# Optimization experiments

Measured on AMD Instinct MI355X. Metric: run time of the kernel, lower is better.

The kernel has to match this reference:

```python
import jax, jax.numpy as jnp
import numpy as np

HEAD_DIM = 128
NUM_QUERY_GROUPS = 4
BLOCK_SIZE = 64
NUM_SELECTED = 16


def setup_inputs() -> dict:
    key = jax.random.key(0)
    k1, k2, k3, k4 = jax.random.split(key, 4)
    query = jax.random.normal(k1, (4, 32, 1, 128), jnp.float32)
    compressed_keys = jax.random.normal(k2, (4, 32, 128, 128), jnp.float32)
    keys = jax.random.normal(k3, (4, 4, 8192, 128), jnp.float32)
    values = jax.random.normal(k4, (4, 4, 8192, 128), jnp.float32)
    return {"query": query, "compressed_keys": compressed_keys, "keys": keys, "values": values}


def reference(query, compressed_keys, keys, values):
    # --- compressed attention importance scores ---
    q = query[:, :, -1, :]                                     # [B, H, D] (last query position)
    scale = 1.0 / (HEAD_DIM ** 0.5)
    scores = jnp.einsum('bhd,bhnd->bhn', q, compressed_keys) * scale  # [B, H, N]
    probs = jax.nn.softmax(scores, axis=-1)
    # --- GQA pooling: mean over heads within each query group ---
    B, H, N = probs.shape
    probs = probs.reshape(B, NUM_QUERY_GROUPS, H // NUM_QUERY_GROUPS, N).mean(axis=2)  # [B, G, N]
    # --- top-k block selection ---
    _, idx = jax.lax.top_k(probs, NUM_SELECTED)                # [B, G, n]
    block_starts = idx * BLOCK_SIZE                            # [B, G, n]
    offsets = jnp.arange(BLOCK_SIZE, dtype=block_starts.dtype)
    gather_idx = (block_starts[..., None] + offsets).reshape(B, NUM_QUERY_GROUPS, NUM_SELECTED * BLOCK_SIZE)  # [B, G, n*bs]
    # --- gather whole K/V blocks ---
    selected_keys = jnp.take_along_axis(keys, gather_idx[..., None], axis=2)    # [B, G, n*bs, D]
    selected_values = jnp.take_along_axis(values, gather_idx[..., None], axis=2)
    return selected_keys, selected_values
```

## Files before the change

kernel.cpp:

```cpp
#include <hip/hip_runtime.h>
#include <math.h>

#define BB   4
#define HH   32
#define GG   4
#define HPG  8
#define DD   128
#define NCK  128
#define SEQ  8192
#define NSEL 16
#define BLK  64

__global__ __launch_bounds__(512, 1) void gemv_exp_kernel(const float* __restrict__ query,
                                                          const float* __restrict__ ck,
                                                          float* __restrict__ e_out,
                                                          float* __restrict__ psum_out) {
    const int blk  = blockIdx.x;
    const int bh   = blk >> 1;
    const int half = blk & 1;
    const int t    = threadIdx.x;
    const int r    = (t >> 3) + half * 64;
    const int sub  = t & 7;
    const int w    = t >> 6;

    __shared__ float q_sh[DD];
    __shared__ float wred[8];

    if (t < DD) q_sh[t] = query[(size_t)bh * DD + t];
    __syncthreads();

    const float4* c4 = (const float4*)(ck + ((size_t)bh * NCK + r) * DD) + sub;
    const float4* q4 = ((const float4*)q_sh) + sub;
    float s = 0.0f;
    #pragma unroll
    for (int i = 0; i < 4; ++i) {
        float4 a = q4[i * 8];
        float4 c = c4[i * 8];
        s += a.x * c.x + a.y * c.y + a.z * c.z + a.w * c.w;
    }
    s += __shfl_xor(s, 1);
    s += __shfl_xor(s, 2);
    s += __shfl_xor(s, 4);

    const float e = expf(s * 0.08838834764831845f);
    if (sub == 0) e_out[(size_t)bh * NCK + r] = e;

    float bsum = e;
    #pragma unroll
    for (int off = 1; off < 64; off <<= 1) bsum += __shfl_xor(bsum, off);
    if ((t & 63) == 0) wred[w] = bsum * 0.125f;
    __syncthreads();

    if (t == 0) {
        float p = 0.0f;
        #pragma unroll
        for (int i = 0; i < 8; ++i) p += wred[i];
        psum_out[bh * 2 + half] = p;
    }
}

__global__ __launch_bounds__(256, 1) void select_gather_kernel(const float* __restrict__ e_in,
                                                               const float* __restrict__ psum,
                                                               const float* __restrict__ keys,
                                                               const float* __restrict__ values,
                                                               float* __restrict__ out) {
    const int bid  = blockIdx.x;
    const int q2   = bid & 3;
    const int isV  = q2 >> 1;
    const int half = q2 & 1;
    const int s    = (bid >> 2) & 15;
    const int bg   = bid >> 6;
    const int b    = bg >> 2;
    const int g    = bg & 3;
    const int t    = threadIdx.x;

    __shared__ float pm[NCK];
    __shared__ int   sel_sh;

    if (t < NCK) {
        const int base = b * HH + g * HPG;
        float p = 0.0f;
        #pragma unroll
        for (int j = 0; j < HPG; ++j) {
            const float ej = e_in[(size_t)(base + j) * NCK + t];
            const float sj = psum[(base + j) * 2] + psum[(base + j) * 2 + 1];
            p += ej / sj;
        }
        pm[t] = p;
    }
    __syncthreads();

    if (t < NCK) {
        const float mv = pm[t];
        int rank = 0;
        for (int i = 0; i < NCK; ++i) {
            const float vi = pm[i];
            if (vi > mv || (vi == mv && i < t)) ++rank;
        }
        if (rank == s) sel_sh = t;
    }
    __syncthreads();
    const int sel = sel_sh;

    const size_t src  = ((size_t)bg * SEQ + (size_t)sel * BLK + half * 32) * DD;
    const size_t dst  = ((size_t)bg * (NSEL * BLK) + (size_t)s * BLK + half * 32) * DD;
    const size_t VOFF = (size_t)BB * GG * NSEL * BLK * DD;

    const float4* sp = (const float4*)((isV ? values : keys) + src);
    float4*       dp = (float4*)(out + (isV ? VOFF : 0) + dst);

    #pragma unroll
    for (int i = 0; i < 4; ++i) dp[i * 256 + t] = sp[i * 256 + t];
}

extern "C" void kernel_launch(void* const* d_in, const int* in_sizes, int n_in,
                              void* d_out, int out_size, void* d_ws, size_t ws_size,
                              hipStream_t stream) {
    const float* query  = (const float*)d_in[0];
    const float* ck     = (const float*)d_in[1];
    const float* keys   = (const float*)d_in[2];
    const float* values = (const float*)d_in[3];
    float* out = (float*)d_out;

    float* e_ws   = (float*)d_ws;
    float* ps_ws  = (float*)((char*)d_ws + (size_t)BB * HH * NCK * sizeof(float));

    gemv_exp_kernel<<<BB * HH * 2, 512, 0, stream>>>(query, ck, e_ws, ps_ws);
    select_gather_kernel<<<BB * GG * NSEL * 4, 256, 0, stream>>>(e_ws, ps_ws, keys, values, out);
}
```

Before: 18.45 us.

## Fuse score and gather kernels with a global atomic grid barrier

```diff
diff --git a/kernel.cpp b/kernel.cpp
--- a/kernel.cpp
+++ b/kernel.cpp
@@ -10,61 +10,72 @@
 #define SEQ  8192
 #define NSEL 16
 #define BLK  64
+#define NPROD 256
 
-__global__ __launch_bounds__(512, 1) void gemv_exp_kernel(const float* __restrict__ query,
-                                                          const float* __restrict__ ck,
-                                                          float* __restrict__ e_out,
-                                                          float* __restrict__ psum_out) {
-    const int blk  = blockIdx.x;
-    const int bh   = blk >> 1;
-    const int half = blk & 1;
-    const int t    = threadIdx.x;
-    const int r    = (t >> 3) + half * 64;
-    const int sub  = t & 7;
-    const int w    = t >> 6;
+__global__ __launch_bounds__(256, 4) void fused_nsa_kernel(
+    const float* __restrict__ query,
+    const float* __restrict__ ck,
+    const float* __restrict__ keys,
+    const float* __restrict__ values,
+    float* __restrict__ e_ws,
+    float* __restrict__ ps_ws,
+    unsigned int* __restrict__ ctr,
+    float* __restrict__ out)
+{
+    const int bid = blockIdx.x;
+    const int t   = threadIdx.x;
 
     __shared__ float q_sh[DD];
-    __shared__ float wred[8];
+    __shared__ float wred[4];
+    __shared__ float pm[NCK];
+    __shared__ int   sel_sh;
 
-    if (t < DD) q_sh[t] = query[(size_t)bh * DD + t];
+    if (bid < NPROD) {
+        const int bh   = bid >> 1;
+        const int half = bid & 1;
+        const int r    = half * 64 + (t >> 2);
+        const int sub  = t & 3;
+        const int w    = t >> 6;
+
+        if (t < DD) q_sh[t] = query[(size_t)bh * DD + t];
+        __syncthreads();
+
+        const float4* c4 = (const float4*)(ck + ((size_t)bh * NCK + r) * DD) + sub;
+        const float4* q4 = ((const float4*)q_sh) + sub;
+        float s = 0.0f;
+        #pragma unroll
+        for (int i = 0; i < 8; ++i) {
+            float4 a = q4[i * 4];
+            float4 c = c4[i * 4];
+            s += a.x * c.x + a.y * c.y + a.z * c.z + a.w * c.w;
+        }
+        s += __shfl_xor(s, 1);
+        s += __shfl_xor(s, 2);
+
+        const float e = expf(s * 0.08838834764831845f);
+        if (sub == 0) e_ws[(size_t)bh * NCK + r] = e;
+
+        float bsum = e;
+        #pragma unroll
+        for (int off = 1; off < 64; off <<= 1) bsum += __shfl_xor(bsum, off);
+        if ((t & 63) == 0) wred[w] = bsum * 0.25f;
+        __syncthreads();
+        if (t == 0)
+            ps_ws[bh * 2 + half] = (wred[0] + wred[1]) + (wred[2] + wred[3]);
+
+        __threadfence();
+        __syncthreads();
+        if (t == 0)
+            __hip_atomic_fetch_add(ctr, 1u, __ATOMIC_RELEASE, __HIP_MEMORY_SCOPE_AGENT);
+    }
+
+    if (t == 0) {
+        while (__hip_atomic_load(ctr, __ATOMIC_RELAXED, __HIP_MEMORY_SCOPE_AGENT) != NPROD)
+            __builtin_amdgcn_s_sleep(2);
+        (void)__hip_atomic_load(ctr, __ATOMIC_ACQUIRE, __HIP_MEMORY_SCOPE_AGENT);
+    }
     __syncthreads();
 
-    const float4* c4 = (const float4*)(ck + ((size_t)bh * NCK + r) * DD) + sub;
-    const float4* q4 = ((const float4*)q_sh) + sub;
-    float s = 0.0f;
-    #pragma unroll
-    for (int i = 0; i < 4; ++i) {
-        float4 a = q4[i * 8];
-        float4 c = c4[i * 8];
-        s += a.x * c.x + a.y * c.y + a.z * c.z + a.w * c.w;
-    }
-    s += __shfl_xor(s, 1);
-    s += __shfl_xor(s, 2);
-    s += __shfl_xor(s, 4);
-
-    const float e = expf(s * 0.08838834764831845f);
-    if (sub == 0) e_out[(size_t)bh * NCK + r] = e;
-
-    float bsum = e;
-    #pragma unroll
-    for (int off = 1; off < 64; off <<= 1) bsum += __shfl_xor(bsum, off);
-    if ((t & 63) == 0) wred[w] = bsum * 0.125f;
-    __syncthreads();
-
-    if (t == 0) {
-        float p = 0.0f;
-        #pragma unroll
-        for (int i = 0; i < 8; ++i) p += wred[i];
-        psum_out[bh * 2 + half] = p;
-    }
-}
-
-__global__ __launch_bounds__(256, 1) void select_gather_kernel(const float* __restrict__ e_in,
-                                                               const float* __restrict__ psum,
-                                                               const float* __restrict__ keys,
-                                                               const float* __restrict__ values,
-                                                               float* __restrict__ out) {
-    const int bid  = blockIdx.x;
     const int q2   = bid & 3;
     const int isV  = q2 >> 1;
     const int half = q2 & 1;
@@ -72,18 +83,14 @@
     const int bg   = bid >> 6;
     const int b    = bg >> 2;
     const int g    = bg & 3;
-    const int t    = threadIdx.x;
-
-    __shared__ float pm[NCK];
-    __shared__ int   sel_sh;
 
     if (t < NCK) {
         const int base = b * HH + g * HPG;
         float p = 0.0f;
         #pragma unroll
         for (int j = 0; j < HPG; ++j) {
-            const float ej = e_in[(size_t)(base + j) * NCK + t];
-            const float sj = psum[(base + j) * 2] + psum[(base + j) * 2 + 1];
+            const float ej = e_ws[(size_t)(base + j) * NCK + t];
+            const float sj = ps_ws[(base + j) * 2] + ps_ws[(base + j) * 2 + 1];
             p += ej / sj;
         }
         pm[t] = p;
@@ -122,9 +129,14 @@
     const float* values = (const float*)d_in[3];
     float* out = (float*)d_out;
 
-    float* e_ws   = (float*)d_ws;
-    float* ps_ws  = (float*)((char*)d_ws + (size_t)BB * HH * NCK * sizeof(float));
+    const size_t OFF_PS  = (size_t)BB * HH * NCK * sizeof(float);
+    const size_t OFF_CTR = OFF_PS + (size_t)BB * HH * 2 * sizeof(float);
 
-    gemv_exp_kernel<<<BB * HH * 2, 512, 0, stream>>>(query, ck, e_ws, ps_ws);
-    select_gather_kernel<<<BB * GG * NSEL * 4, 256, 0, stream>>>(e_ws, ps_ws, keys, values, out);
+    float*        e_ws  = (float*)d_ws;
+    float*        ps_ws = (float*)((char*)d_ws + OFF_PS);
+    unsigned int* ctr   = (unsigned int*)((char*)d_ws + OFF_CTR);
+
+    hipMemsetAsync(ctr, 0, sizeof(unsigned int), stream);
+    fused_nsa_kernel<<<BB * GG * NSEL * 4, 256, 0, stream>>>(query, ck, keys, values,
+                                                             e_ws, ps_ws, ctr, out);
 }
```

Result: slower. 56.62 us (+206.9%).
